# Performance work log

Measured on AMD Instinct MI355X. Metric: run time of the kernel, lower is better.

## Reference

```python
import jax, jax.numpy as jnp
import numpy as np

XY, Zs, V = 32, 16, 10000
N = XY * XY * Zs            # 16384 states
B, T, L = 32, 64, 16
# neighbor offsets from transition_log_p: (x,y,z) -> x + XY*(y + XY*z)
OFFS = np.array([0, 1, -1, XY, -XY, XY * XY, 2 * XY * XY], dtype=np.int64)
NBR = (np.arange(N)[:, None] - OFFS[None, :]) % N   # [N,7] source-state index per neighbor


def setup_inputs() -> dict:
    key = jax.random.key(0)
    k1, k2, k3, k4 = jax.random.split(key, 4)
    return {
        "stories_tensor": jax.random.randint(k1, (B, T, L), 0, V),
        "story_length": T,
        "length": L,
        "trans_unnorm": jax.random.normal(k2, (N, 7), dtype=jnp.float32),
        "emis_unnorm": jax.random.normal(k3, (N, V), dtype=jnp.float32),
        "prior_unnorm": jax.random.normal(k4, (N,), dtype=jnp.float32),
    }


def reference(stories_tensor, story_length, length, trans_unnorm, emis_unnorm, prior_unnorm):
    logT = jax.nn.log_softmax(trans_unnorm, axis=-1)     # [N,7]
    logE = jax.nn.log_softmax(emis_unnorm, axis=1)       # [N,V]
    logpi = jax.nn.log_softmax(prior_unnorm, axis=0)     # [N]
    nbr = jnp.asarray(NBR)                               # [N,7]

    def emit(tokens):                                    # [B,L] -> [B,N]
        # emission_log_p: logE[:, tokens] -> [N,B,L], sum over words, transpose
        return jnp.swapaxes(logE[:, tokens].sum(-1), 0, 1)

    scores0 = emit(stories_tensor[:, 0]) + logpi[None, :]   # [B,N]

    def step(scores, tokens):
        em = emit(tokens)                                # [B,N]
        prev = scores[:, nbr]                            # [B,N,7] gather of prior alpha
        new = em + jax.scipy.special.logsumexp(logT[None, :, :] + prev, axis=-1)
        return new, None

    seq = jnp.swapaxes(stories_tensor, 0, 1)[1:]         # [T-1,B,L]
    scores, _ = jax.lax.scan(step, scores0, seq)
    return jax.scipy.special.logsumexp(scores, axis=-1)  # [B]
```

## Files before the change

### kernel.cpp

```cpp
#include <hip/hip_runtime.h>
#include <hip/hip_bf16.h>
#include <stdint.h>

#define XY 32
#define ZS 16
#define NST 16384
#define NMASK 16383
#define VOC 10000
#define BB 32
#define TT 64
#define LL 16

#define LOG2E 1.4426950408889634f
#define LN2F  0.6931471805599453f

__device__ __forceinline__ float fexp2(float x) {
#if __has_builtin(__builtin_amdgcn_exp2f)
  return __builtin_amdgcn_exp2f(x);
#else
  return exp2f(x);
#endif
}
__device__ __forceinline__ float flog2(float x) {
#if __has_builtin(__builtin_amdgcn_logf)
  return __builtin_amdgcn_logf(x);
#else
  return log2f(x);
#endif
}

__device__ __forceinline__ float waveMax(float v) {
  #pragma unroll
  for (int o = 32; o >= 1; o >>= 1) v = fmaxf(v, __shfl_xor(v, o, 64));
  return v;
}
__device__ __forceinline__ float waveSum(float v) {
  #pragma unroll
  for (int o = 32; o >= 1; o >>= 1) v += __shfl_xor(v, o, 64);
  return v;
}

__global__ __launch_bounds__(256) void tok_conv(const int* __restrict__ st,
                                                unsigned short* __restrict__ tok16) {
  int i = blockIdx.x * 256 + threadIdx.x;
  if (i >= BB * TT * LL) return;
  int l = i & 15;
  int tb = i >> 4;
  int b = tb & 31;
  int t = tb >> 5;
  tok16[i] = (unsigned short)st[b * (TT * LL) + t * LL + l];
}

__global__ __launch_bounds__(256) void prep_trans(const float* __restrict__ tr,
                                                  float* __restrict__ Tn) {
  int n = blockIdx.x * 256 + threadIdx.x;
  if (n >= NST) return;
  float v[7];
  float m = -3.4e38f;
  #pragma unroll
  for (int k = 0; k < 7; ++k) { v[k] = tr[n * 7 + k]; m = fmaxf(m, v[k]); }
  float s = 0.f;
  #pragma unroll
  for (int k = 0; k < 7; ++k) { v[k] = fexp2((v[k] - m) * LOG2E); s += v[k]; }
  float inv = 1.0f / s;
  #pragma unroll
  for (int k = 0; k < 7; ++k) Tn[n * 8 + k] = v[k] * inv;
  Tn[n * 8 + 7] = 0.f;
}

__global__ __launch_bounds__(256) void emis_kernel(const float* __restrict__ emis,
                                                   const unsigned short* __restrict__ tok16,
                                                   float* __restrict__ em) {
  const int n = blockIdx.x;
  const int tid = threadIdx.x;
  __shared__ float row[VOC];
  __shared__ float sred[8];

  const float4* rp = (const float4*)(emis + (size_t)n * VOC);
  float4 regs[10];
  float lmax = -3.4e38f;
  #pragma unroll
  for (int it = 0; it < 10; ++it) {
    int i = tid + it * 256;
    if (i < VOC / 4) {
      float4 v = rp[i];
      regs[it] = v;
      ((float4*)row)[i] = v;
      lmax = fmaxf(lmax, fmaxf(fmaxf(v.x, v.y), fmaxf(v.z, v.w)));
    }
  }
  float wm = waveMax(lmax);
  if ((tid & 63) == 0) sred[tid >> 6] = wm;
  __syncthreads();
  float bm = fmaxf(fmaxf(sred[0], sred[1]), fmaxf(sred[2], sred[3]));

  float ls = 0.f;
  #pragma unroll
  for (int it = 0; it < 10; ++it) {
    int i = tid + it * 256;
    if (i < VOC / 4) {
      float4 v = regs[it];
      ls += fexp2((v.x - bm) * LOG2E);
      ls += fexp2((v.y - bm) * LOG2E);
      ls += fexp2((v.z - bm) * LOG2E);
      ls += fexp2((v.w - bm) * LOG2E);
    }
  }
  float wsum = waveSum(ls);
  if ((tid & 63) == 0) sred[4 + (tid >> 6)] = wsum;
  __syncthreads();
  float lse = bm + flog2(sred[4] + sred[5] + sred[6] + sred[7]) * LN2F;
  float sub = (float)LL * lse;

  for (int i = tid; i < TT * BB; i += 256) {
    const uint4* tp = (const uint4*)(tok16 + (size_t)i * 16);
    uint4 w0 = tp[0];
    uint4 w1 = tp[1];
    float s = row[w0.x & 0xFFFF] + row[w0.x >> 16]
            + row[w0.y & 0xFFFF] + row[w0.y >> 16]
            + row[w0.z & 0xFFFF] + row[w0.z >> 16]
            + row[w0.w & 0xFFFF] + row[w0.w >> 16]
            + row[w1.x & 0xFFFF] + row[w1.x >> 16]
            + row[w1.y & 0xFFFF] + row[w1.y >> 16]
            + row[w1.z & 0xFFFF] + row[w1.z >> 16]
            + row[w1.w & 0xFFFF] + row[w1.w >> 16];
    em[(size_t)n * (TT * BB) + i] = s - sub;
  }
}

__global__ __launch_bounds__(256) void init_kernel(const float* __restrict__ em,
                                                   const float* __restrict__ prior,
                                                   float* __restrict__ s0) {
  int idx = blockIdx.x * 256 + threadIdx.x;
  int n = idx >> 5, b = idx & 31;
  s0[idx] = em[((size_t)n << 11) + b] + prior[n];
}

__global__ __launch_bounds__(256) void step_kernel(const float* __restrict__ sp,
                                                   float* __restrict__ sn,
                                                   const float* __restrict__ em_t,
                                                   const float* __restrict__ Tn) {
  int idx = blockIdx.x * 256 + threadIdx.x;
  int n = idx >> 5, b = idx & 31;
  float p0 = sp[idx];
  float p1 = sp[(((n - 1) & NMASK) << 5) | b];
  float p2 = sp[(((n + 1) & NMASK) << 5) | b];
  float p3 = sp[(((n - 32) & NMASK) << 5) | b];
  float p4 = sp[(((n + 32) & NMASK) << 5) | b];
  float p5 = sp[(((n - 1024) & NMASK) << 5) | b];
  float p6 = sp[(((n - 2048) & NMASK) << 5) | b];
  const float4* t4 = (const float4*)(Tn + ((size_t)n << 3));
  float4 ta = t4[0];
  float4 tb = t4[1];
  float m = fmaxf(p0, fmaxf(fmaxf(p1, p2), fmaxf(fmaxf(p3, p4), fmaxf(p5, p6))));
  float s = ta.x * fexp2((p0 - m) * LOG2E)
          + ta.y * fexp2((p1 - m) * LOG2E)
          + ta.z * fexp2((p2 - m) * LOG2E)
          + ta.w * fexp2((p3 - m) * LOG2E)
          + tb.x * fexp2((p4 - m) * LOG2E)
          + tb.y * fexp2((p5 - m) * LOG2E)
          + tb.z * fexp2((p6 - m) * LOG2E);
  sn[idx] = em_t[((size_t)n << 11) + b] + m + flog2(s) * LN2F;
}

__global__ __launch_bounds__(256) void final_kernel(const float* __restrict__ sf,
                                                    const float* __restrict__ prior,
                                                    float* __restrict__ out) {
  int b = blockIdx.x;
  int tid = threadIdx.x;
  __shared__ float sred[8];

  float lmax = -3.4e38f;
  for (int n = tid; n < NST; n += 256) lmax = fmaxf(lmax, sf[(n << 5) + b]);
  float wm = waveMax(lmax);
  if ((tid & 63) == 0) sred[tid >> 6] = wm;
  __syncthreads();
  float bm = fmaxf(fmaxf(sred[0], sred[1]), fmaxf(sred[2], sred[3]));
  float ls = 0.f;
  for (int n = tid; n < NST; n += 256) ls += fexp2((sf[(n << 5) + b] - bm) * LOG2E);
  float wsum = waveSum(ls);
  if ((tid & 63) == 0) sred[4 + (tid >> 6)] = wsum;
  __syncthreads();
  float lse_s = bm + flog2(sred[4] + sred[5] + sred[6] + sred[7]) * LN2F;

  __syncthreads();
  float pmax = -3.4e38f;
  for (int n = tid; n < NST; n += 256) pmax = fmaxf(pmax, prior[n]);
  float wpm = waveMax(pmax);
  if ((tid & 63) == 0) sred[tid >> 6] = wpm;
  __syncthreads();
  float pm = fmaxf(fmaxf(sred[0], sred[1]), fmaxf(sred[2], sred[3]));
  float ps = 0.f;
  for (int n = tid; n < NST; n += 256) ps += fexp2((prior[n] - pm) * LOG2E);
  float wps = waveSum(ps);
  if ((tid & 63) == 0) sred[4 + (tid >> 6)] = wps;
  __syncthreads();
  float lse_p = pm + flog2(sred[4] + sred[5] + sred[6] + sred[7]) * LN2F;

  if (tid == 0) out[b] = lse_s - lse_p;
}

extern "C" void kernel_launch(void* const* d_in, const int* in_sizes, int n_in,
                              void* d_out, int out_size, void* d_ws, size_t ws_size,
                              hipStream_t stream) {
  const int* stories  = (const int*)d_in[0];
  const float* trans  = (const float*)d_in[3];
  const float* emis   = (const float*)d_in[4];
  const float* prior  = (const float*)d_in[5];
  float* out = (float*)d_out;

  char* ws = (char*)d_ws;
  float* em = (float*)ws;
  float* sA = (float*)(ws + (size_t)NST * TT * BB * 4);
  float* sB = sA + (size_t)NST * BB;
  float* Tn = sB + (size_t)NST * BB;
  unsigned short* tok16 = (unsigned short*)(Tn + (size_t)NST * 8);

  tok_conv<<<(BB * TT * LL + 255) / 256, 256, 0, stream>>>(stories, tok16);
  prep_trans<<<(NST + 255) / 256, 256, 0, stream>>>(trans, Tn);
  emis_kernel<<<NST, 256, 0, stream>>>(emis, tok16, em);
  init_kernel<<<(NST * BB) / 256, 256, 0, stream>>>(em, prior, sA);

  float* cur = sA;
  float* nxt = sB;
  for (int t = 1; t < TT; ++t) {
    step_kernel<<<(NST * BB) / 256, 256, 0, stream>>>(cur, nxt, em + (size_t)t * BB, Tn);
    float* tmp = cur; cur = nxt; nxt = tmp;
  }
  final_kernel<<<BB, 256, 0, stream>>>(cur, prior, out);
}
```

Baseline: 1.219 ms.

## Fuse HMM forward recursion into one persistent LDS-resident kernel per batch

Replaces 63 per-timestep step launches, plus the init and final kernels, with a single kernel of one 1024-thread block per batch element. That block keeps the full alpha vector in double-buffered LDS with wrap-around halos, and reuses the z-neighbour values it already holds in registers across its unrolled iterations. Emissions are prescaled to log2, and a new transpose kernel makes each timestep's emissions contiguous per batch. The prior log-sum-exp moves into its own small kernel. This removes launch overhead and the strided global gathers of alpha. In exchange it uses only 32 CUs, needs about 131KB of LDS per block, adds a transpose pass over the emission table, and re-reads the transition table every step.

Result: slower. 1.488 ms (+22.1%).

```diff
diff --git a/kernel.cpp b/kernel.cpp
--- a/kernel.cpp
+++ b/kernel.cpp
@@ -1,5 +1,4 @@
 #include <hip/hip_runtime.h>
-#include <hip/hip_bf16.h>
 #include <stdint.h>
 
 #define XY 32
@@ -10,6 +9,8 @@
 #define BB 32
 #define TT 64
 #define LL 16
+#define HALO 32
+#define BUFSZ (NST + 2 * HALO)
 
 #define LOG2E 1.4426950408889634f
 #define LN2F  0.6931471805599453f
@@ -66,6 +67,25 @@
   #pragma unroll
   for (int k = 0; k < 7; ++k) Tn[n * 8 + k] = v[k] * inv;
   Tn[n * 8 + 7] = 0.f;
+}
+
+__global__ __launch_bounds__(256) void lse_prior(const float* __restrict__ prior,
+                                                 float* __restrict__ lse_p) {
+  int tid = threadIdx.x;
+  __shared__ float sred[8];
+  float lmax = -3.4e38f;
+  for (int n = tid; n < NST; n += 256) lmax = fmaxf(lmax, prior[n]);
+  float wm = waveMax(lmax);
+  if ((tid & 63) == 0) sred[tid >> 6] = wm;
+  __syncthreads();
+  float bm = fmaxf(fmaxf(sred[0], sred[1]), fmaxf(sred[2], sred[3]));
+  float ls = 0.f;
+  for (int n = tid; n < NST; n += 256) ls += fexp2((prior[n] - bm) * LOG2E);
+  float ws = waveSum(ls);
+  if ((tid & 63) == 0) sred[4 + (tid >> 6)] = ws;
+  __syncthreads();
+  if (tid == 0)
+    lse_p[0] = bm + flog2(sred[4] + sred[5] + sred[6] + sred[7]) * LN2F;
 }
 
 __global__ __launch_bounds__(256) void emis_kernel(const float* __restrict__ emis,
@@ -124,80 +144,112 @@
             + row[w1.y & 0xFFFF] + row[w1.y >> 16]
             + row[w1.z & 0xFFFF] + row[w1.z >> 16]
             + row[w1.w & 0xFFFF] + row[w1.w >> 16];
-    em[(size_t)n * (TT * BB) + i] = s - sub;
-  }
-}
-
-__global__ __launch_bounds__(256) void init_kernel(const float* __restrict__ em,
-                                                   const float* __restrict__ prior,
-                                                   float* __restrict__ s0) {
-  int idx = blockIdx.x * 256 + threadIdx.x;
-  int n = idx >> 5, b = idx & 31;
-  s0[idx] = em[((size_t)n << 11) + b] + prior[n];
-}
-
-__global__ __launch_bounds__(256) void step_kernel(const float* __restrict__ sp,
-                                                   float* __restrict__ sn,
-                                                   const float* __restrict__ em_t,
-                                                   const float* __restrict__ Tn) {
-  int idx = blockIdx.x * 256 + threadIdx.x;
-  int n = idx >> 5, b = idx & 31;
-  float p0 = sp[idx];
-  float p1 = sp[(((n - 1) & NMASK) << 5) | b];
-  float p2 = sp[(((n + 1) & NMASK) << 5) | b];
-  float p3 = sp[(((n - 32) & NMASK) << 5) | b];
-  float p4 = sp[(((n + 32) & NMASK) << 5) | b];
-  float p5 = sp[(((n - 1024) & NMASK) << 5) | b];
-  float p6 = sp[(((n - 2048) & NMASK) << 5) | b];
-  const float4* t4 = (const float4*)(Tn + ((size_t)n << 3));
-  float4 ta = t4[0];
-  float4 tb = t4[1];
-  float m = fmaxf(p0, fmaxf(fmaxf(p1, p2), fmaxf(fmaxf(p3, p4), fmaxf(p5, p6))));
-  float s = ta.x * fexp2((p0 - m) * LOG2E)
-          + ta.y * fexp2((p1 - m) * LOG2E)
-          + ta.z * fexp2((p2 - m) * LOG2E)
-          + ta.w * fexp2((p3 - m) * LOG2E)
-          + tb.x * fexp2((p4 - m) * LOG2E)
-          + tb.y * fexp2((p5 - m) * LOG2E)
-          + tb.z * fexp2((p6 - m) * LOG2E);
-  sn[idx] = em_t[((size_t)n << 11) + b] + m + flog2(s) * LN2F;
-}
-
-__global__ __launch_bounds__(256) void final_kernel(const float* __restrict__ sf,
-                                                    const float* __restrict__ prior,
-                                                    float* __restrict__ out) {
-  int b = blockIdx.x;
-  int tid = threadIdx.x;
-  __shared__ float sred[8];
-
-  float lmax = -3.4e38f;
-  for (int n = tid; n < NST; n += 256) lmax = fmaxf(lmax, sf[(n << 5) + b]);
-  float wm = waveMax(lmax);
-  if ((tid & 63) == 0) sred[tid >> 6] = wm;
-  __syncthreads();
-  float bm = fmaxf(fmaxf(sred[0], sred[1]), fmaxf(sred[2], sred[3]));
+    em[(size_t)n * (TT * BB) + i] = (s - sub) * LOG2E;
+  }
+}
+
+__global__ __launch_bounds__(256) void transpose_em(const float* __restrict__ em,
+                                                    float* __restrict__ em2) {
+  __shared__ float tile[64][65];
+  const int i0 = blockIdx.x * 64;
+  const int n0 = blockIdx.y * 64;
+  const int tx = threadIdx.x & 63;
+  const int ty = threadIdx.x >> 6;
+  #pragma unroll
+  for (int r = 0; r < 16; ++r) {
+    int nr = ty + 4 * r;
+    tile[nr][tx] = em[(size_t)(n0 + nr) * (TT * BB) + i0 + tx];
+  }
+  __syncthreads();
+  #pragma unroll
+  for (int r = 0; r < 16; ++r) {
+    int ir = ty + 4 * r;
+    em2[(size_t)(i0 + ir) * NST + n0 + tx] = tile[tx][ir];
+  }
+}
+
+__global__ __launch_bounds__(1024) void recursion_kernel(const float* __restrict__ em2,
+                                                         const float* __restrict__ Tn8,
+                                                         const float* __restrict__ prior,
+                                                         const float* __restrict__ lse_p,
+                                                         float* __restrict__ out) {
+  extern __shared__ float lds[];
+  float* buf0 = lds;
+  float* buf1 = lds + BUFSZ;
+  const int b = blockIdx.x;
+  const int tid = threadIdx.x;
+
+  {
+    const float* e0 = em2 + ((size_t)b << 14);
+    #pragma unroll
+    for (int s = 0; s < 16; ++s) {
+      int n = tid + (s << 10);
+      float v = e0[n] + prior[n] * LOG2E;
+      buf0[HALO + n] = v;
+      if (n < HALO) buf0[HALO + NST + n] = v;
+      if (n >= NST - HALO) buf0[n - (NST - HALO)] = v;
+    }
+  }
+  __syncthreads();
+
+  for (int t = 1; t < TT; ++t) {
+    const float* prev = (t & 1) ? buf0 : buf1;
+    float* cur = (t & 1) ? buf1 : buf0;
+    const float* e = em2 + ((size_t)(t * BB + b) << 14);
+    float pm1 = prev[HALO + ((tid - 1024) & NMASK)];
+    float pm2 = prev[HALO + ((tid - 2048) & NMASK)];
+    #pragma unroll
+    for (int s = 0; s < 16; ++s) {
+      int n = tid + (s << 10);
+      float p0 = prev[HALO + n];
+      float a1 = prev[HALO + n - 1];
+      float a2 = prev[HALO + n + 1];
+      float a3 = prev[HALO + n - 32];
+      float a4 = prev[HALO + n + 32];
+      float p5 = pm1;
+      float p6 = pm2;
+      const float4* tp = (const float4*)(Tn8 + ((size_t)n << 3));
+      float4 ta = tp[0];
+      float4 tb = tp[1];
+      float m = fmaxf(fmaxf(fmaxf(p0, a1), fmaxf(a2, a3)),
+                      fmaxf(fmaxf(a4, p5), p6));
+      float ssum = ta.x * fexp2(p0 - m) + ta.y * fexp2(a1 - m)
+                 + ta.z * fexp2(a2 - m) + ta.w * fexp2(a3 - m)
+                 + tb.x * fexp2(a4 - m) + tb.y * fexp2(p5 - m)
+                 + tb.z * fexp2(p6 - m);
+      float v = e[n] + m + flog2(ssum);
+      cur[HALO + n] = v;
+      if (n < HALO) cur[HALO + NST + n] = v;
+      if (n >= NST - HALO) cur[n - (NST - HALO)] = v;
+      pm2 = pm1;
+      pm1 = p0;
+    }
+    __syncthreads();
+  }
+
+  float lm = -3.4e38f;
+  #pragma unroll
+  for (int s = 0; s < 16; ++s)
+    lm = fmaxf(lm, buf1[HALO + tid + (s << 10)]);
+  lm = waveMax(lm);
+  if ((tid & 63) == 0) buf0[tid >> 6] = lm;
+  __syncthreads();
+  float bm = buf0[0];
+  #pragma unroll
+  for (int k = 1; k < 16; ++k) bm = fmaxf(bm, buf0[k]);
   float ls = 0.f;
-  for (int n = tid; n < NST; n += 256) ls += fexp2((sf[(n << 5) + b] - bm) * LOG2E);
-  float wsum = waveSum(ls);
-  if ((tid & 63) == 0) sred[4 + (tid >> 6)] = wsum;
-  __syncthreads();
-  float lse_s = bm + flog2(sred[4] + sred[5] + sred[6] + sred[7]) * LN2F;
-
-  __syncthreads();
-  float pmax = -3.4e38f;
-  for (int n = tid; n < NST; n += 256) pmax = fmaxf(pmax, prior[n]);
-  float wpm = waveMax(pmax);
-  if ((tid & 63) == 0) sred[tid >> 6] = wpm;
-  __syncthreads();
-  float pm = fmaxf(fmaxf(sred[0], sred[1]), fmaxf(sred[2], sred[3]));
-  float ps = 0.f;
-  for (int n = tid; n < NST; n += 256) ps += fexp2((prior[n] - pm) * LOG2E);
-  float wps = waveSum(ps);
-  if ((tid & 63) == 0) sred[4 + (tid >> 6)] = wps;
-  __syncthreads();
-  float lse_p = pm + flog2(sred[4] + sred[5] + sred[6] + sred[7]) * LN2F;
-
-  if (tid == 0) out[b] = lse_s - lse_p;
+  #pragma unroll
+  for (int s = 0; s < 16; ++s)
+    ls += fexp2(buf1[HALO + tid + (s << 10)] - bm);
+  ls = waveSum(ls);
+  if ((tid & 63) == 0) buf0[16 + (tid >> 6)] = ls;
+  __syncthreads();
+  if (tid == 0) {
+    float s = 0.f;
+    #pragma unroll
+    for (int k = 0; k < 16; ++k) s += buf0[16 + k];
+    out[b] = LN2F * (bm + flog2(s)) - lse_p[0];
+  }
 }
 
 extern "C" void kernel_launch(void* const* d_in, const int* in_sizes, int n_in,
@@ -210,22 +262,20 @@
   float* out = (float*)d_out;
 
   char* ws = (char*)d_ws;
-  float* em = (float*)ws;
-  float* sA = (float*)(ws + (size_t)NST * TT * BB * 4);
-  float* sB = sA + (size_t)NST * BB;
-  float* Tn = sB + (size_t)NST * BB;
+  float* em  = (float*)ws;
+  float* em2 = em + (size_t)NST * TT * BB;
+  float* Tn  = em2 + (size_t)NST * TT * BB;
   unsigned short* tok16 = (unsigned short*)(Tn + (size_t)NST * 8);
+  float* lse_p = (float*)(tok16 + (size_t)BB * TT * LL);
 
   tok_conv<<<(BB * TT * LL + 255) / 256, 256, 0, stream>>>(stories, tok16);
-  prep_trans<<<(NST + 255) / 256, 256, 0, stream>>>(trans, Tn);
+  prep_trans<<<NST / 256, 256, 0, stream>>>(trans, Tn);
+  lse_prior<<<1, 256, 0, stream>>>(prior, lse_p);
   emis_kernel<<<NST, 256, 0, stream>>>(emis, tok16, em);
-  init_kernel<<<(NST * BB) / 256, 256, 0, stream>>>(em, prior, sA);
-
-  float* cur = sA;
-  float* nxt = sB;
-  for (int t = 1; t < TT; ++t) {
-    step_kernel<<<(NST * BB) / 256, 256, 0, stream>>>(cur, nxt, em + (size_t)t * BB, Tn);
-    float* tmp = cur; cur = nxt; nxt = tmp;
-  }
-  final_kernel<<<BB, 256, 0, stream>>>(cur, prior, out);
-}
+  transpose_em<<<dim3(TT * BB / 64, NST / 64), 256, 0, stream>>>(em, em2);
+
+  size_t dynlds = (size_t)2 * BUFSZ * sizeof(float);
+  hipFuncSetAttribute((const void*)recursion_kernel,
+                      hipFuncAttributeMaxDynamicSharedMemorySize, (int)dynlds);
+  recursion_kernel<<<BB, 1024, dynlds, stream>>>(em2, Tn, prior, lse_p, out);
+}
```
